# Kernel tuning notes

Measured on AMD Instinct MI355X. Metric: run time of the kernel, lower is better.

The kernel has to match this reference:

```python
import jax, jax.numpy as jnp
import numpy as np


def _make_grid(h, w):
    """Replicates gen_grid_coordinates_optimized(h, w, stride=1) vectorized in numpy.
    Returns (h*3, w*3, 2) float32 grid in grid_sample convention (x=col, y=row, in [-1,1])."""
    pi = np.pi
    dphi = pi / h
    dtheta = 2 * pi / w
    tp, tt, icp = np.tan(dphi), np.tan(dtheta), 1.0 / np.cos(dphi)
    xys = np.array([[(-tt, icp * tp), (0, tp), (tt, icp * tp)],
                    [(-tt, 0), (1, 1), (tt, 0)],
                    [(-tt, -icp * tp), (0, -tp), (tt, -icp * tp)]], dtype=np.float64)
    xk, yk = xys[..., 0], xys[..., 1]          # (3,3) kernel offsets on tangent plane
    rho = np.sqrt(xk ** 2 + yk ** 2)
    v = np.arctan(rho)
    cv, sv = np.cos(v), np.sin(v)
    rr = np.arange(h, dtype=np.float64)
    cc = np.arange(w, dtype=np.float64)
    phi = -((rr + 0.5) / h * pi - pi / 2)      # (h,)
    theta = (cc + 0.5) / w * 2 * pi - pi       # (w,)
    cph = np.cos(phi)[:, None, None]
    sph = np.sin(phi)[:, None, None]
    # (h,3,3) ; clip guards fp roundoff at poles (mathematically |arg|<=1)
    new_phi = np.arcsin(np.clip(cv * sph + yk * sv * cph / rho, -1.0, 1.0))
    dtheta_off = np.arctan(xk * sv / (rho * cph * cv - yk * sph * sv))  # (h,3,3)
    new_theta = theta[None, :, None, None] + dtheta_off[:, None]        # (h,w,3,3)
    new_r = np.broadcast_to(((-new_phi + pi / 2) * h / pi - 0.5)[:, None], (h, w, 3, 3)).copy()
    new_c = (new_theta + pi) * w / (2 * pi) - 0.5
    new_c = (new_c + w) % w
    # kernel center samples the pixel itself
    new_r[:, :, 1, 1] = rr[:, None]
    new_c[:, :, 1, 1] = cc[None, :]
    gy = new_r * 2 / h - 1
    gx = new_c * 2 / w - 1
    grid = np.stack([gx, gy], axis=-1)                      # (h,w,ki,kj,2)
    grid = grid.transpose(0, 2, 1, 3, 4).reshape(h * 3, w * 3, 2)
    return grid.astype(np.float32)


def _grid_sample_bilinear(x, grid):
    """F.grid_sample(mode='bilinear', align_corners=True, padding_mode='zeros').
    x: (N,C,H,W), grid: (Hg,Wg,2) shared across batch. Returns (N,C,Hg,Wg)."""
    N, C, H, W = x.shape
    ix = (grid[..., 0] + 1) * 0.5 * (W - 1)
    iy = (grid[..., 1] + 1) * 0.5 * (H - 1)
    x0 = jnp.floor(ix)
    y0 = jnp.floor(iy)
    x1, y1 = x0 + 1, y0 + 1
    xflat = x.reshape(N, C, H * W)

    def corner(yc, xc, wgt):
        valid = (xc >= 0) & (xc <= W - 1) & (yc >= 0) & (yc <= H - 1)
        xi = jnp.clip(xc, 0, W - 1).astype(jnp.int32)
        yi = jnp.clip(yc, 0, H - 1).astype(jnp.int32)
        idx = (yi * W + xi).reshape(-1)
        v = xflat[:, :, idx].reshape(N, C, *xc.shape)
        return v * (wgt * valid)[None, None]

    out = (corner(y0, x0, (x1 - ix) * (y1 - iy))
           + corner(y0, x1, (ix - x0) * (y1 - iy))
           + corner(y1, x0, (x1 - ix) * (iy - y0))
           + corner(y1, x1, (ix - x0) * (iy - y0)))
    return out


def setup_inputs() -> dict:
    key = jax.random.key(0)
    k1, k2 = jax.random.split(key)
    B, Cin, Cout, H, W = 4, 16, 32, 256, 512
    x = jax.random.normal(k1, (B, Cin, H, W), dtype=jnp.float32)
    fan_out = Cout * 9  # kaiming_normal fan_out, relu gain
    weight = jax.random.normal(k2, (Cout, Cin, 3, 3), dtype=jnp.float32) * np.sqrt(2.0 / fan_out)
    bias = jnp.zeros((Cout,), dtype=jnp.float32)
    grid = jnp.asarray(_make_grid(H, W))  # (H*3, W*3, 2) constant spherical warp
    return {"x": x, "weight": weight, "bias": bias, "grid": grid}


def reference(x, weight, bias, grid):
    s = _grid_sample_bilinear(x, grid)  # (N,C,3H,3W)
    out = jax.lax.conv_general_dilated(
        s, weight, window_strides=(3, 3), padding='VALID',
        dimension_numbers=('NCHW', 'OIHW', 'NCHW'))
    return out + bias[None, :, None, None]
```

## Files before the change

kernel.cpp:

```cpp
#include <hip/hip_runtime.h>

#define HH 256
#define WW 512
#define NCIN 16
#define NCOUT 32
#define NB 4

typedef _Float16 half8 __attribute__((ext_vector_type(8)));
typedef float f32x16 __attribute__((ext_vector_type(16)));

#define XT_OFF   0u
#define WFRAG_OFF 16777216u
#define YTAB_OFF  (16777216u + 16384u)
#define WS_NEED   (YTAB_OFF + 36864u)

__global__ __launch_bounds__(256) void precompute_all(const float* __restrict__ x,
                                                      const float* __restrict__ w,
                                                      const float* __restrict__ grid,
                                                      _Float16* __restrict__ xh,
                                                      _Float16* __restrict__ wfrag,
                                                      float4* __restrict__ ytab) {
    const float2* g2 = reinterpret_cast<const float2*>(grid);
    if (blockIdx.x < 2048) {
        const int lb = (blockIdx.x & 7) * 256 + (blockIdx.x >> 3);
        const int t = lb * 256 + threadIdx.x;
        const int c = t & (WW - 1);
        const int r = (t >> 9) & (HH - 1);
        const int b = t >> 17;
        const float* xp = x + ((size_t)(b * NCIN) * HH + r) * WW + c;
        half8 h0, h1;
#pragma unroll
        for (int ci = 0; ci < 8; ++ci)  h0[ci] = (_Float16)xp[(size_t)ci * (HH * WW)];
#pragma unroll
        for (int ci = 0; ci < 8; ++ci)  h1[ci] = (_Float16)xp[(size_t)(8 + ci) * (HH * WW)];
        half8* op = reinterpret_cast<half8*>(xh) + (size_t)t * 2;
        op[0] = h0;
        op[1] = h1;
        return;
    }
    if (blockIdx.x < 2066) {
        const int e = (blockIdx.x - 2048) * 256 + threadIdx.x;
        if (e < 4608) {
            const int j = e & 7, lane = (e >> 3) & 63, t = e >> 9;
            const int c32 = lane & 31, h = lane >> 5;
            wfrag[e] = (_Float16)w[c32 * 144 + (h * 8 + j) * 9 + t];
        }
        return;
    }
    const int u = (blockIdx.x - 2066) * 256 + threadIdx.x;
    if (u < HH * 9) {
        const int r = u / 9, tap = u - r * 9;
        const int kr = tap / 3, kc = tap - kr * 3;
        const float gy = g2[(size_t)(r * 3 + kr) * 1536 + kc].y;
        const float iy = ((gy + 1.0f) * 0.5f) * (float)(HH - 1);
        const float y0f = floorf(iy);
        const float fy = iy - y0f;
        const int y0 = (int)y0f, y1 = y0 + 1;
        float wy0 = 1.0f - fy, wy1 = fy;
        if (y0 < 0 || y0 > HH - 1) wy0 = 0.0f;
        if (y1 < 0 || y1 > HH - 1) wy1 = 0.0f;
        const int cy0 = min(max(y0, 0), HH - 1), cy1 = min(max(y1, 0), HH - 1);
        ytab[u] = make_float4(wy0, wy1, __int_as_float(cy0), __int_as_float(cy1));
    }
}

__global__ __launch_bounds__(256, 4) void sphere_mfma_kernel(const _Float16* __restrict__ xh,
                                                             const float* __restrict__ grid,
                                                             const _Float16* __restrict__ wfrag,
                                                             const float4* __restrict__ ytab,
                                                             const float* __restrict__ bias,
                                                             float* __restrict__ out) {
    const int tid = threadIdx.x, lane = tid & 63, wv = tid >> 6;
    const int c32 = lane & 31, h = lane >> 5;
    const int px = wv * 32 + c32;

    const int lb = ((blockIdx.x & 7) << 9) + (blockIdx.x >> 3);
    const int pixbase = lb << 7;
    const int b    = pixbase >> 17;
    const int rimg = (pixbase >> 9) & (HH - 1);
    const int c0   = pixbase & (WW - 1);

    float wy0s[9], wy1s[9];
    int Rb0[9], Rb1[9];
#pragma unroll
    for (int t = 0; t < 9; ++t) {
        const float4 y = ytab[rimg * 9 + t];
        wy0s[t] = y.x;
        wy1s[t] = y.y;
        Rb0[t] = (b * HH + __float_as_int(y.z)) << 10;
        Rb1[t] = (b * HH + __float_as_int(y.w)) << 10;
    }

    const float2* g2 = reinterpret_cast<const float2*>(grid);
    const float2* grow = g2 + (size_t)(rimg * 3) * 1536 + (size_t)(c0 + px) * 3;
    float fxs[9];
    int x0s[9];
#pragma unroll
    for (int kr = 0; kr < 3; ++kr)
#pragma unroll
        for (int kc = 0; kc < 3; ++kc) {
            const float gx = grow[(size_t)kr * 1536 + kc].x;
            const float ix = ((gx + 1.0f) * 0.5f) * (float)(WW - 1);
            const float x0f = floorf(ix);
            fxs[kr * 3 + kc] = ix - x0f;
            x0s[kr * 3 + kc] = (int)x0f;
        }

    const half8* wf8 = reinterpret_cast<const half8*>(wfrag);
    half8 wA[9];
#pragma unroll
    for (int t = 0; t < 9; ++t) wA[t] = wf8[t * 64 + lane];

    const half8* x8 = reinterpret_cast<const half8*>(xh);
    f32x16 acc = {};

    half8 A00a, A01a, A10a, A11a, A00b, A01b, A10b, A11b;

#define GLOAD(tt, S)                                                     \
    {                                                                    \
        const int p0_ = Rb0[tt] + (x0s[tt] << 1) + h;                    \
        const int p1_ = Rb1[tt] + (x0s[tt] << 1) + h;                    \
        A00##S = x8[p0_];                                                \
        A01##S = x8[p0_ + 2];                                            \
        A10##S = x8[p1_];                                                \
        A11##S = x8[p1_ + 2];                                            \
    }

#define CONSUME(tt, S)                                                   \
    {                                                                    \
        const float fx_ = fxs[tt];                                       \
        const float wx0_ = 1.0f - fx_;                                   \
        const float w00_ = wx0_ * wy0s[tt], w01_ = fx_ * wy0s[tt];       \
        const float w10_ = wx0_ * wy1s[tt], w11_ = fx_ * wy1s[tt];       \
        const _Float16 W00_ = (_Float16)w00_, W01_ = (_Float16)w01_;     \
        const _Float16 W10_ = (_Float16)w10_, W11_ = (_Float16)w11_;     \
        const half8 B00_ = {W00_, W00_, W00_, W00_, W00_, W00_, W00_, W00_}; \
        const half8 B01_ = {W01_, W01_, W01_, W01_, W01_, W01_, W01_, W01_}; \
        const half8 B10_ = {W10_, W10_, W10_, W10_, W10_, W10_, W10_, W10_}; \
        const half8 B11_ = {W11_, W11_, W11_, W11_, W11_, W11_, W11_, W11_}; \
        half8 pk_ = A00##S * B00_;                                       \
        pk_ += A01##S * B01_;                                            \
        pk_ += A10##S * B10_;                                            \
        pk_ += A11##S * B11_;                                            \
        acc = __builtin_amdgcn_mfma_f32_32x32x16_f16(wA[tt], pk_, acc, 0, 0, 0); \
    }

    GLOAD(0, a)
    GLOAD(1, b)
    CONSUME(0, a) GLOAD(2, a)
    CONSUME(1, b) GLOAD(3, b)
    CONSUME(2, a) GLOAD(4, a)
    CONSUME(3, b) GLOAD(5, b)
    CONSUME(4, a) GLOAD(6, a)
    CONSUME(5, b) GLOAD(7, b)
    CONSUME(6, a) GLOAD(8, a)
    CONSUME(7, b)
    CONSUME(8, a)
#undef GLOAD
#undef CONSUME

    const int pix = c0 + wv * 32 + c32;
    float* ob = out + (((size_t)(b * NCOUT) * HH + rimg) * WW) + pix;
#pragma unroll
    for (int reg = 0; reg < 16; ++reg) {
        const int co = (reg & 3) + 8 * (reg >> 2) + 4 * h;
        ob[(size_t)co * (HH * WW)] = acc[reg] + bias[co];
    }
}

__global__ __launch_bounds__(256) void sphere_conv_fallback(const float* __restrict__ x,
                                                            const float* __restrict__ weight,
                                                            const float* __restrict__ bias,
                                                            const float* __restrict__ grid,
                                                            float* __restrict__ out) {
    __shared__ float wlds[NCIN * 9 * NCOUT];
    const int tid = threadIdx.x;
    for (int e = tid; e < NCIN * 9 * NCOUT; e += 256) {
        const int co  = e & (NCOUT - 1);
        const int cik = e >> 5;
        wlds[e] = weight[co * (NCIN * 9) + cik];
    }
    __syncthreads();

    const int pindex = blockIdx.x * 256 + tid;
    const int c = pindex & (WW - 1);
    const int r = (pindex >> 9) & (HH - 1);
    const int b = pindex >> 17;

    float acc[NCOUT];
#pragma unroll
    for (int o = 0; o < NCOUT; ++o) acc[o] = 0.0f;

    const float2* g2 = reinterpret_cast<const float2*>(grid);

#pragma unroll 1
    for (int k = 0; k < 9; ++k) {
        const int kr = k / 3, kc = k - kr * 3;
        const float2 g = g2[(r * 3 + kr) * (WW * 3) + (c * 3 + kc)];
        const float ix = ((g.x + 1.0f) * 0.5f) * (float)(WW - 1);
        const float iy = ((g.y + 1.0f) * 0.5f) * (float)(HH - 1);
        const float x0f = floorf(ix), y0f = floorf(iy);
        const float fx = ix - x0f, fy = iy - y0f;
        const int x0 = (int)x0f, y0 = (int)y0f;
        const int x1 = x0 + 1, y1 = y0 + 1;
        float wx0 = 1.0f - fx, wx1 = fx, wy0 = 1.0f - fy, wy1 = fy;
        if (x0 < 0 || x0 > WW - 1) wx0 = 0.0f;
        if (x1 < 0 || x1 > WW - 1) wx1 = 0.0f;
        if (y0 < 0 || y0 > HH - 1) wy0 = 0.0f;
        if (y1 < 0 || y1 > HH - 1) wy1 = 0.0f;
        const int cx0 = min(max(x0, 0), WW - 1), cx1 = min(max(x1, 0), WW - 1);
        const int cy0 = min(max(y0, 0), HH - 1), cy1 = min(max(y1, 0), HH - 1);
        const float w00 = wx0 * wy0, w01 = wx1 * wy0, w10 = wx0 * wy1, w11 = wx1 * wy1;

#pragma unroll 1
        for (int ci = 0; ci < NCIN; ++ci) {
            const float* xb = x + (size_t)((b * NCIN + ci) * HH) * WW;
            const float a00 = xb[cy0 * WW + cx0];
            const float a01 = xb[cy0 * WW + cx1];
            const float a10 = xb[cy1 * WW + cx0];
            const float a11 = xb[cy1 * WW + cx1];
            const float s = w00 * a00 + w01 * a01 + w10 * a10 + w11 * a11;
            const float4* wl = reinterpret_cast<const float4*>(&wlds[(ci * 9 + k) * NCOUT]);
#pragma unroll
            for (int o = 0; o < 8; ++o) {
                const float4 wv = wl[o];
                acc[o * 4 + 0] += wv.x * s;
                acc[o * 4 + 1] += wv.y * s;
                acc[o * 4 + 2] += wv.z * s;
                acc[o * 4 + 3] += wv.w * s;
            }
        }
    }

    const int obase = ((b * NCOUT) * HH + r) * WW + c;
#pragma unroll
    for (int o = 0; o < NCOUT; ++o) {
        out[obase + o * (HH * WW)] = acc[o] + bias[o];
    }
}

extern "C" void kernel_launch(void* const* d_in, const int* in_sizes, int n_in,
                              void* d_out, int out_size, void* d_ws, size_t ws_size,
                              hipStream_t stream) {
    const float* x    = (const float*)d_in[0];
    const float* w    = (const float*)d_in[1];
    const float* bias = (const float*)d_in[2];
    const float* grid = (const float*)d_in[3];
    float* out = (float*)d_out;

    if (ws_size >= WS_NEED) {
        char* ws = (char*)d_ws;
        _Float16* xh    = (_Float16*)(ws + XT_OFF);
        _Float16* wfrag = (_Float16*)(ws + WFRAG_OFF);
        float4*   ytab  = (float4*)(ws + YTAB_OFF);

        precompute_all<<<2075, 256, 0, stream>>>(x, w, grid, xh, wfrag, ytab);
        sphere_mfma_kernel<<<4096, 256, 0, stream>>>(xh, grid, wfrag, ytab, bias, out);
    } else {
        sphere_conv_fallback<<<2048, 256, 0, stream>>>(x, w, bias, grid, out);
    }
}
```

Before: 46.53 us.

## Stage gathered input rows into LDS via async global_load_lds double buffering

```diff
diff --git a/kernel.cpp b/kernel.cpp
--- a/kernel.cpp
+++ b/kernel.cpp
@@ -8,6 +8,9 @@
 
 typedef _Float16 half8 __attribute__((ext_vector_type(8)));
 typedef float f32x16 __attribute__((ext_vector_type(16)));
+
+typedef const __attribute__((address_space(1))) void gvoid_t;
+typedef __attribute__((address_space(3))) void lvoid_t;
 
 #define XT_OFF   0u
 #define WFRAG_OFF 16777216u
@@ -70,6 +73,7 @@
                                                              const float4* __restrict__ ytab,
                                                              const float* __restrict__ bias,
                                                              float* __restrict__ out) {
+    __shared__ _Float16 Sl[4][2][2][640];
     const int tid = threadIdx.x, lane = tid & 63, wv = tid >> 6;
     const int c32 = lane & 31, h = lane >> 5;
     const int px = wv * 32 + c32;
@@ -111,52 +115,74 @@
 #pragma unroll
     for (int t = 0; t < 9; ++t) wA[t] = wf8[t * 64 + lane];
 
-    const half8* x8 = reinterpret_cast<const half8*>(xh);
+    const char* xbase = reinterpret_cast<const char*>(xh);
     f32x16 acc = {};
-
-    half8 A00a, A01a, A10a, A11a, A00b, A01b, A10b, A11b;
-
-#define GLOAD(tt, S)                                                     \
-    {                                                                    \
-        const int p0_ = Rb0[tt] + (x0s[tt] << 1) + h;                    \
-        const int p1_ = Rb1[tt] + (x0s[tt] << 1) + h;                    \
-        A00##S = x8[p0_];                                                \
-        A01##S = x8[p0_ + 2];                                            \
-        A10##S = x8[p1_];                                                \
-        A11##S = x8[p1_ + 2];                                            \
-    }
-
-#define CONSUME(tt, S)                                                   \
-    {                                                                    \
-        const float fx_ = fxs[tt];                                       \
-        const float wx0_ = 1.0f - fx_;                                   \
-        const float w00_ = wx0_ * wy0s[tt], w01_ = fx_ * wy0s[tt];       \
-        const float w10_ = wx0_ * wy1s[tt], w11_ = fx_ * wy1s[tt];       \
-        const _Float16 W00_ = (_Float16)w00_, W01_ = (_Float16)w01_;     \
-        const _Float16 W10_ = (_Float16)w10_, W11_ = (_Float16)w11_;     \
-        const half8 B00_ = {W00_, W00_, W00_, W00_, W00_, W00_, W00_, W00_}; \
-        const half8 B01_ = {W01_, W01_, W01_, W01_, W01_, W01_, W01_, W01_}; \
-        const half8 B10_ = {W10_, W10_, W10_, W10_, W10_, W10_, W10_, W10_}; \
-        const half8 B11_ = {W11_, W11_, W11_, W11_, W11_, W11_, W11_, W11_}; \
-        half8 pk_ = A00##S * B00_;                                       \
-        pk_ += A01##S * B01_;                                            \
-        pk_ += A10##S * B10_;                                            \
-        pk_ += A11##S * B11_;                                            \
-        acc = __builtin_amdgcn_mfma_f32_32x32x16_f16(wA[tt], pk_, acc, 0, 0, 0); \
-    }
-
-    GLOAD(0, a)
-    GLOAD(1, b)
-    CONSUME(0, a) GLOAD(2, a)
-    CONSUME(1, b) GLOAD(3, b)
-    CONSUME(2, a) GLOAD(4, a)
-    CONSUME(3, b) GLOAD(5, b)
-    CONSUME(4, a) GLOAD(6, a)
-    CONSUME(5, b) GLOAD(7, b)
-    CONSUME(6, a) GLOAD(8, a)
-    CONSUME(7, b)
-    CONSUME(8, a)
-#undef GLOAD
+    int xfs[9];
+
+#define ISSUE(tt)                                                                  \
+    {                                                                              \
+        __builtin_amdgcn_sched_barrier(0);                                         \
+        const int xf_ = __builtin_amdgcn_readfirstlane(x0s[tt]);                   \
+        xfs[tt] = xf_;                                                             \
+        const size_t rb0_ = ((size_t)(unsigned)Rb0[tt]) << 4;                      \
+        const size_t rb1_ = ((size_t)(unsigned)Rb1[tt]) << 4;                      \
+        const int pu1_ = (xf_ - 2 + (lane >> 1)) & 511;                            \
+        const size_t o1_ = (size_t)(pu1_ * 32 + (lane & 1) * 16);                  \
+        _Float16* db_ = &Sl[wv][(tt) & 1][0][0];                                   \
+        __builtin_amdgcn_global_load_lds((gvoid_t*)(xbase + rb0_ + o1_),           \
+                                         (lvoid_t*)db_, 16, 0, 0);                 \
+        __builtin_amdgcn_global_load_lds((gvoid_t*)(xbase + rb1_ + o1_),           \
+                                         (lvoid_t*)(db_ + 640), 16, 0, 0);         \
+        if (lane < 16) {                                                           \
+            const int pu2_ = (xf_ - 2 + ((64 + lane) >> 1)) & 511;                 \
+            const size_t o2_ = (size_t)(pu2_ * 32 + (lane & 1) * 16);              \
+            __builtin_amdgcn_global_load_lds((gvoid_t*)(xbase + rb0_ + o2_),       \
+                                             (lvoid_t*)(db_ + 512), 16, 0, 0);     \
+            __builtin_amdgcn_global_load_lds((gvoid_t*)(xbase + rb1_ + o2_),       \
+                                             (lvoid_t*)(db_ + 640 + 512), 16, 0, 0); \
+        }                                                                          \
+    }
+
+#define CONSUME(tt, VM)                                                            \
+    {                                                                              \
+        asm volatile("s_waitcnt vmcnt(" VM ")" ::: "memory");                      \
+        __builtin_amdgcn_sched_barrier(0);                                         \
+        const int rel_ = (x0s[tt] - xfs[tt] + 2) & 511;                            \
+        const _Float16* rb_ = &Sl[wv][(tt) & 1][0][0];                             \
+        const int s0_ = (2 * rel_ + h) * 8;                                        \
+        const half8 A00 = *reinterpret_cast<const half8*>(rb_ + s0_);              \
+        const half8 A01 = *reinterpret_cast<const half8*>(rb_ + s0_ + 16);         \
+        const half8 A10 = *reinterpret_cast<const half8*>(rb_ + 640 + s0_);        \
+        const half8 A11 = *reinterpret_cast<const half8*>(rb_ + 640 + s0_ + 16);   \
+        const float fx_ = fxs[tt];                                                 \
+        const float wx0_ = 1.0f - fx_;                                             \
+        const float w00_ = wx0_ * wy0s[tt], w01_ = fx_ * wy0s[tt];                 \
+        const float w10_ = wx0_ * wy1s[tt], w11_ = fx_ * wy1s[tt];                 \
+        const _Float16 W00_ = (_Float16)w00_, W01_ = (_Float16)w01_;               \
+        const _Float16 W10_ = (_Float16)w10_, W11_ = (_Float16)w11_;               \
+        const half8 B00_ = {W00_, W00_, W00_, W00_, W00_, W00_, W00_, W00_};       \
+        const half8 B01_ = {W01_, W01_, W01_, W01_, W01_, W01_, W01_, W01_};       \
+        const half8 B10_ = {W10_, W10_, W10_, W10_, W10_, W10_, W10_, W10_};       \
+        const half8 B11_ = {W11_, W11_, W11_, W11_, W11_, W11_, W11_, W11_};       \
+        half8 pk_ = A00 * B00_;                                                    \
+        pk_ += A01 * B01_;                                                         \
+        pk_ += A10 * B10_;                                                         \
+        pk_ += A11 * B11_;                                                         \
+        acc = __builtin_amdgcn_mfma_f32_32x32x16_f16(wA[tt], pk_, acc, 0, 0, 0);   \
+    }
+
+    ISSUE(0)
+    ISSUE(1)
+    CONSUME(0, "4") ISSUE(2)
+    CONSUME(1, "4") ISSUE(3)
+    CONSUME(2, "4") ISSUE(4)
+    CONSUME(3, "4") ISSUE(5)
+    CONSUME(4, "4") ISSUE(6)
+    CONSUME(5, "4") ISSUE(7)
+    CONSUME(6, "4") ISSUE(8)
+    CONSUME(7, "4")
+    CONSUME(8, "0")
+#undef ISSUE
 #undef CONSUME
 
     const int pix = c0 + wv * 32 + c32;
```

Result: no change. 47.40 us (+1.9%).
